# Optimization experiments

Hardware: AMD Instinct MI355X
Metric: run time of the kernel (lower is better)

## Reference

```python
import jax, jax.numpy as jnp
import numpy as np

K = 8                      # batch_k
NONZERO_CUTOFF = 1.4       # nonzero_loss_cutoff
MARGIN = 1.0               # F.triplet_margin_loss default (module's margin arg is unused)
PD_EPS = 1e-6              # torch pairwise_distance eps


def setup_inputs() -> dict:
    key = jax.random.key(0)
    x = jax.random.normal(key, (4096, 128), dtype=jnp.float32)
    return {"x": x}


def _sample_indices(x, key):
    """Distance-weighted negative sampling; returns (a_idx, p_idx, n_idx), each [n*(K-1)]."""
    n, d = x.shape
    # per-row L2 normalize (eps added to norm, as in original)
    xn = x / (jnp.sqrt(jnp.sum(x * x, axis=1, keepdims=True)) + 1e-5)
    # pairwise euclidean distance; identity added under sqrt exactly as original
    sq = jnp.sum(xn * xn, axis=1, keepdims=True)               # [n,1]
    dist2 = sq + sq.T - 2.0 * (xn @ xn.T)                       # [n,n]
    dist = jnp.sqrt(dist2 + jnp.eye(n, dtype=x.dtype))          # [n,n]
    # distance-weighted sampling log-weights (Wu et al.)
    log_w = (2.0 - d) * jnp.log(dist) - (d - 3) / 2.0 * jnp.log(1.0 - 0.25 * dist * dist)
    w = jnp.exp(log_w - jnp.max(log_w))
    # block mask: same-block pairs excluded
    block = jnp.arange(n) // K                                  # [n]
    mask = (block[:, None] != block[None, :]).astype(x.dtype)
    w = w * mask * (dist < NONZERO_CUTOFF).astype(x.dtype)
    row_sum = jnp.sum(w, axis=1, keepdims=True)
    # rows where weights are degenerate fall back to uniform (original's try/except)
    valid = jnp.isfinite(row_sum) & (row_sum > 0) & jnp.all(jnp.isfinite(w), axis=1, keepdims=True)
    logits = jnp.where(valid, jnp.where(w > 0, jnp.log(w), -jnp.inf), 0.0)   # [n,n]
    # batched categorical sampling via Gumbel-max: K-1 negatives per anchor
    g = jax.random.gumbel(key, (n, K - 1, n), dtype=jnp.float32)
    n_idx = jnp.argmax(logits[:, None, :] + g, axis=-1).reshape(-1)          # [n*(K-1)]
    # anchor/positive pairs: for each i, all other members of its block
    r = jnp.arange(n) % K                                       # position in block
    off = jnp.arange(K - 1)
    p_off = jnp.where(off[None, :] < r[:, None], off[None, :], off[None, :] + 1)
    p_idx = (block[:, None] * K + p_off).reshape(-1)            # [n*(K-1)]
    a_idx = jnp.repeat(jnp.arange(n), K - 1)                    # [n*(K-1)]
    return a_idx, p_idx, n_idx


def reference(x) -> jnp.ndarray:
    key = jax.random.key(42)
    a_idx, p_idx, n_idx = _sample_indices(x, key)
    a, p, ng = x[a_idx], x[p_idx], x[n_idx]
    d_ap = jnp.sqrt(jnp.sum((a - p + PD_EPS) ** 2, axis=1))
    d_an = jnp.sqrt(jnp.sum((a - ng + PD_EPS) ** 2, axis=1))
    return jnp.mean(jnp.maximum(d_ap - d_an + MARGIN, 0.0))
```

## Files before the change

kernel.cpp:

```cpp
#include <hip/hip_runtime.h>
#include <stdint.h>

#define NROWS 4096
#define DIM   128
#define KB    8
#define NS    7
#define TCH   16
#define NSEG  4
#define NPAIR 2048
#define HALF_CNT 58720256u

typedef __bf16 v8bf __attribute__((ext_vector_type(8)));
typedef float  v4f  __attribute__((ext_vector_type(4)));

__device__ __forceinline__ uint32_t rotl32(uint32_t x, int r) {
    return (x << r) | (x >> (32 - r));
}

__device__ __forceinline__ void threefry2x32(uint32_t c0, uint32_t c1,
                                             uint32_t& o0, uint32_t& o1) {
    const uint32_t ks0 = 0u;
    const uint32_t ks1 = 42u;
    const uint32_t ks2 = 0x1BD11BDAu ^ ks0 ^ ks1;
    uint32_t x0 = c0 + ks0;
    uint32_t x1 = c1 + ks1;
#define TF_R(r) { x0 += x1; x1 = rotl32(x1, r); x1 ^= x0; }
    TF_R(13) TF_R(15) TF_R(26) TF_R(6)
    x0 += ks1; x1 += ks2 + 1u;
    TF_R(17) TF_R(29) TF_R(16) TF_R(24)
    x0 += ks2; x1 += ks0 + 2u;
    TF_R(13) TF_R(15) TF_R(26) TF_R(6)
    x0 += ks0; x1 += ks1 + 3u;
    TF_R(17) TF_R(29) TF_R(16) TF_R(24)
    x0 += ks1; x1 += ks2 + 4u;
    TF_R(13) TF_R(15) TF_R(26) TF_R(6)
    x0 += ks2; x1 += ks0 + 5u;
#undef TF_R
    o0 = x0; o1 = x1;
}

__device__ __forceinline__ float gumbel_of(uint32_t b) {
    float f = __uint_as_float((b >> 9) | 0x3f800000u) - 1.0f;
    float u = f + 1.17549435e-38f;
    float l1 = __log2f(u);
    float inner = -0.69314718055994531f * l1;
    float l2 = __log2f(inner);
    return -0.69314718055994531f * l2;
}

__global__ void knorm(const float* __restrict__ x, __bf16* __restrict__ xb,
                      float* __restrict__ sqv) {
    const int i = blockIdx.x;
    const int t = threadIdx.x;
    float2 v = ((const float2*)(x + (size_t)i * DIM))[t];
    float s = v.x * v.x + v.y * v.y;
#pragma unroll
    for (int m = 32; m > 0; m >>= 1) s += __shfl_xor(s, m, 64);
    float norm = sqrtf(s) + 1e-5f;
    float ox = v.x / norm, oy = v.y / norm;
    union { __bf16 b[2]; uint32_t u; } ph;
    ph.b[0] = (__bf16)ox; ph.b[1] = (__bf16)oy;
    ((uint32_t*)xb)[i * 64 + t] = ph.u;
    float s2 = ox * ox + oy * oy;
#pragma unroll
    for (int m = 32; m > 0; m >>= 1) s2 += __shfl_xor(s2, m, 64);
    if (t == 0) sqv[i] = s2;
}

__global__ __launch_bounds__(256, 4) void kdist(
        const __bf16* __restrict__ xb, const float* __restrict__ sqv,
        int* __restrict__ cnt, unsigned short* __restrict__ t16,
        float2* __restrict__ nwp) {
    const int lane  = threadIdx.x & 63;
    const int chunk = (blockIdx.x << 2) + (threadIdx.x >> 6);
    const int grp   = blockIdx.y;
    const int rlo = lane & 15;
    const int khi = lane >> 4;
    const unsigned int below = (1u << rlo) - 1u;

    const int afr = grp * 8 + (rlo >> 1) + ((rlo & 1) << 11);
    v8bf ah[4];
#pragma unroll
    for (int ks = 0; ks < 4; ++ks)
        ah[ks] = *(const v8bf*)(xb + (size_t)afr * DIM + ks * 32 + khi * 8);

    const int base = grp * 8 + khi * 2;
    float sqA[4];
    sqA[0] = sqv[base];
    sqA[1] = sqv[base + 2048];
    sqA[2] = sqv[base + 1];
    sqA[3] = sqv[base + 2049];

    const int rbA = ((base)     * 16 + chunk) << 8;
    const int rbB = ((base + 1) * 16 + chunk) << 8;
    unsigned int cA = 0, cB = 0;

    const int tcol0 = chunk * 256 + rlo;

    v8bf bhn[4];
    float sqn;
    {
        const size_t boff = (size_t)tcol0 * DIM + khi * 8;
#pragma unroll
        for (int ks = 0; ks < 4; ++ks) bhn[ks] = *(const v8bf*)(xb + boff + ks * 32);
        sqn = sqv[tcol0];
    }

#pragma unroll 1
    for (int cg = 0; cg < 16; ++cg) {
        v8bf bhc[4];
#pragma unroll
        for (int ks = 0; ks < 4; ++ks) bhc[ks] = bhn[ks];
        const float sqB = sqn;
        const int tcol = tcol0 + cg * 16;

        if (cg < 15) {
            const size_t boff = (size_t)(tcol + 16) * DIM + khi * 8;
#pragma unroll
            for (int ks = 0; ks < 4; ++ks) bhn[ks] = *(const v8bf*)(xb + boff + ks * 32);
            sqn = sqv[tcol + 16];
        }

        v4f acc = {0.f, 0.f, 0.f, 0.f};
#pragma unroll
        for (int ks = 0; ks < 4; ++ks)
            acc = __builtin_amdgcn_mfma_f32_16x16x32_bf16(ah[ks], bhc[ks], acc, 0, 0, 0);

        const int tBlk = tcol >> 3;
        const bool bd0 = (tBlk != grp);
        const bool bd1 = (tBlk != grp + 256);

        float nw[4];
        bool  ic[4];
#pragma unroll
        for (int q = 0; q < 4; ++q) {
            float d2  = fmaf(-2.0f, acc[q], sqA[q] + sqB);
            float l1  = __log2f(d2);
            float t2  = fmaf(-0.25f, d2, 1.0f);
            float l2  = __log2f(t2);
            float wiv = exp2f(fmaf(63.0f, l1, 62.5f * l2));
            bool incl = (d2 < 1.96f) && ((q & 1) ? bd1 : bd0);
            ic[q] = incl;
            nw[q] = incl ? -wiv : -INFINITY;
        }

        const bool uA = ic[0] | ic[1];
        const bool uB = ic[2] | ic[3];
        unsigned long long ballA = __ballot(uA);
        unsigned long long ballB = __ballot(uB);
        unsigned int subA = (unsigned int)((ballA >> (khi * 16)) & 0xFFFFull);
        unsigned int subB = (unsigned int)((ballB >> (khi * 16)) & 0xFFFFull);
        if (uA) {
            int slot = rbA + (int)cA + __popc(subA & below);
            t16[slot] = (unsigned short)tcol;
            nwp[slot] = make_float2(nw[0], nw[1]);
        }
        if (uB) {
            int slot = rbB + (int)cB + __popc(subB & below);
            t16[slot] = (unsigned short)tcol;
            nwp[slot] = make_float2(nw[2], nw[3]);
        }
        cA += (unsigned int)__popc(subA);
        cB += (unsigned int)__popc(subB);
    }

    if (rlo == 0) {
        cnt[base * 16 + chunk]       = (int)cA;
        cnt[(base + 1) * 16 + chunk] = (int)cB;
    }
}

#define TFR4(r)                                                         \
    _Pragma("unroll") for (int k = 0; k < 4; ++k) {                     \
        x0[k] += x1[k]; x1[k] = rotl32(x1[k], (r)); x1[k] ^= x0[k];     \
    }
#define INJ4(a, b)                                                      \
    _Pragma("unroll") for (int k = 0; k < 4; ++k) {                     \
        x0[k] += (a); x1[k] += (b);                                     \
    }

__global__ __launch_bounds__(256, 4) void kgum(
        const int* __restrict__ cnt, const unsigned short* __restrict__ t16,
        const float2* __restrict__ nwp,
        float* __restrict__ pV, int* __restrict__ pI) {
    const int p    = blockIdx.x;
    const int tid  = threadIdx.x;
    const int seg  = tid >> 6;
    const int lane = tid & 63;
    const int j    = lane & 7;
    const int eo   = lane >> 3;
    const bool jv  = (j < 7);
    const uint32_t pb = ((uint32_t)p * 7u + (uint32_t)j) << 12;

    float bkA = INFINITY, bkB = INFINITY;
    int   btA = 0x7FFFFFFF, btB = 0x7FFFFFFF;

#pragma unroll 1
    for (int c = seg * 4; c < seg * 4 + 4; ++c) {
        const int n  = cnt[p * 16 + c];
        const int rb = (p * 16 + c) << 8;
        int e = eo;

#pragma unroll 1
        for (; e + 24 < n; e += 32) {
            uint32_t tt[4];
            float2   nw[4];
#pragma unroll
            for (int k = 0; k < 4; ++k) {
                tt[k] = t16[rb + e + 8 * k];
                nw[k] = nwp[rb + e + 8 * k];
            }
            uint32_t x0[4], x1[4];
#pragma unroll
            for (int k = 0; k < 4; ++k) {
                uint32_t L = pb + tt[k];
                x0[k] = L;
                x1[k] = L + (HALF_CNT + 42u);
            }
            TFR4(13) TFR4(15) TFR4(26) TFR4(6)
            INJ4(42u, 0x1BD11BF0u + 1u)
            TFR4(17) TFR4(29) TFR4(16) TFR4(24)
            INJ4(0x1BD11BF0u, 2u)
            TFR4(13) TFR4(15) TFR4(26) TFR4(6)
            INJ4(0u, 45u)
            TFR4(17) TFR4(29) TFR4(16) TFR4(24)
            INJ4(42u, 0x1BD11BF0u + 4u)
            TFR4(13) TFR4(15) TFR4(26) TFR4(6)
            INJ4(0x1BD11BF0u, 5u)
#pragma unroll
            for (int k = 0; k < 4; ++k) {
                float fA = __uint_as_float((x0[k] >> 9) | 0x3f800000u) - 1.0f;
                float fB = __uint_as_float((x1[k] >> 9) | 0x3f800000u) - 1.0f;
                float l1A = __log2f(fA + 1.17549435e-38f);
                float l1B = __log2f(fB + 1.17549435e-38f);
                float kA = jv ? l1A * nw[k].x : INFINITY;
                float kB = jv ? l1B * nw[k].y : INFINITY;
                const int ti = (int)tt[k];
                if (kA < bkA || (kA == bkA && ti < btA)) { bkA = kA; btA = ti; }
                if (kB < bkB || (kB == bkB && ti < btB)) { bkB = kB; btB = ti; }
            }
        }

#pragma unroll 1
        for (; e < n; e += 8) {
            const uint32_t t = t16[rb + e];
            const float2 nw  = nwp[rb + e];
            const uint32_t L = pb + t;
            uint32_t o0, o1;
            threefry2x32(L, L + HALF_CNT, o0, o1);
            float fA = __uint_as_float((o0 >> 9) | 0x3f800000u) - 1.0f;
            float fB = __uint_as_float((o1 >> 9) | 0x3f800000u) - 1.0f;
            float l1A = __log2f(fA + 1.17549435e-38f);
            float l1B = __log2f(fB + 1.17549435e-38f);
            float kA = jv ? l1A * nw.x : INFINITY;
            float kB = jv ? l1B * nw.y : INFINITY;
            const int ti = (int)t;
            if (kA < bkA || (kA == bkA && ti < btA)) { bkA = kA; btA = ti; }
            if (kB < bkB || (kB == bkB && ti < btB)) { bkB = kB; btB = ti; }
        }
    }

#pragma unroll
    for (int m = 8; m < 64; m <<= 1) {
        float v2 = __shfl_xor(bkA, m, 64);
        int   t2 = __shfl_xor(btA, m, 64);
        if (v2 < bkA || (v2 == bkA && t2 < btA)) { bkA = v2; btA = t2; }
        v2 = __shfl_xor(bkB, m, 64);
        t2 = __shfl_xor(btB, m, 64);
        if (v2 < bkB || (v2 == bkB && t2 < btB)) { bkB = v2; btB = t2; }
    }

    if (lane < NS) {
        size_t s0 = ((size_t)p * NS + lane) * NSEG + seg;
        pV[s0] = bkA; pI[s0] = btA;
        size_t s1 = ((size_t)(p + 2048) * NS + lane) * NSEG + seg;
        pV[s1] = bkB; pI[s1] = btB;
    }
}

__global__ void kcombine(const float* __restrict__ pV, const int* __restrict__ pI,
                         int* __restrict__ nidx, int nc) {
    int s = blockIdx.x * 256 + threadIdx.x;
    if (s >= NROWS * NS) return;
    float bv = INFINITY;
    int bi = 0x7FFFFFFF;
    for (int c = 0; c < nc; ++c) {
        float v = pV[(size_t)s * nc + c];
        int idx = pI[(size_t)s * nc + c];
        if (v < bv || (v == bv && idx < bi)) { bv = v; bi = idx; }
    }
    nidx[s] = (bv == INFINITY) ? -1 : bi;
}

__global__ __launch_bounds__(256, 2) void ksample(
        const __bf16* __restrict__ xb, const float* __restrict__ sqv,
        float* __restrict__ pV, int* __restrict__ pI) {
    const int lane  = threadIdx.x & 63;
    const int chunk = (blockIdx.x << 2) + (threadIdx.x >> 6);
    const int grp   = blockIdx.y;
    const int rlo = lane & 15;
    const int khi = lane >> 4;

    const int afr = grp * 8 + (rlo >> 1) + ((rlo & 1) << 11);
    v8bf ah[4];
#pragma unroll
    for (int ks = 0; ks < 4; ++ks)
        ah[ks] = *(const v8bf*)(xb + (size_t)afr * DIM + ks * 32 + khi * 8);
    const int base = grp * 8 + khi * 2;
    float sqA[4];
    sqA[0] = sqv[base];
    sqA[1] = sqv[base + 2048];
    sqA[2] = sqv[base + 1];
    sqA[3] = sqv[base + 2049];
    const uint32_t P0 = (uint32_t)base;
    const uint32_t P1 = (uint32_t)(base + 1);

    float    bestV[4][NS];
    uint32_t bestP[4];
#pragma unroll
    for (int q = 0; q < 4; ++q) {
        bestP[q] = 0u;
#pragma unroll
        for (int j = 0; j < NS; ++j) bestV[q][j] = INFINITY;
    }
    const int tcol0 = chunk * 256 + rlo;

    v8bf bhn[4];
    float sqn;
    {
        const size_t boff = (size_t)tcol0 * DIM + khi * 8;
#pragma unroll
        for (int ks = 0; ks < 4; ++ks) bhn[ks] = *(const v8bf*)(xb + boff + ks * 32);
        sqn = sqv[tcol0];
    }

#pragma unroll 1
    for (int cg = 0; cg < 16; ++cg) {
        v8bf bhc[4];
#pragma unroll
        for (int ks = 0; ks < 4; ++ks) bhc[ks] = bhn[ks];
        const float sqB = sqn;
        const int tcol = tcol0 + cg * 16;
        if (cg < 15) {
            const size_t boff = (size_t)(tcol + 16) * DIM + khi * 8;
#pragma unroll
            for (int ks = 0; ks < 4; ++ks) bhn[ks] = *(const v8bf*)(xb + boff + ks * 32);
            sqn = sqv[tcol + 16];
        }
        v4f acc = {0.f, 0.f, 0.f, 0.f};
#pragma unroll
        for (int ks = 0; ks < 4; ++ks)
            acc = __builtin_amdgcn_mfma_f32_16x16x32_bf16(ah[ks], bhc[ks], acc, 0, 0, 0);
        const int tBlk = tcol >> 3;
        const bool bd0 = (tBlk != grp);
        const bool bd1 = (tBlk != grp + 256);
        float nw[4];
#pragma unroll
        for (int q = 0; q < 4; ++q) {
            float d2  = fmaf(-2.0f, acc[q], sqA[q] + sqB);
            float l1  = __log2f(d2);
            float t2  = fmaf(-0.25f, d2, 1.0f);
            float l2  = __log2f(t2);
            float wiv = exp2f(fmaf(63.0f, l1, 62.5f * l2));
            bool incl = (d2 < 1.96f) && ((q & 1) ? bd1 : bd0);
            nw[q] = incl ? -wiv : -INFINITY;
        }
        const uint32_t tB = (uint32_t)tcol;
#pragma unroll
        for (int j = 0; j < NS; ++j) {
            uint32_t L0 = ((P0 * 7u + (uint32_t)j) << 12) + tB;
            uint32_t L1 = ((P1 * 7u + (uint32_t)j) << 12) + tB;
            uint32_t o0, o1, o2, o3;
            threefry2x32(L0, L0 + HALF_CNT, o0, o1);
            threefry2x32(L1, L1 + HALF_CNT, o2, o3);
            float vv[4];
            vv[0] = __log2f(__uint_as_float((o0 >> 9) | 0x3f800000u) - 1.0f + 1.17549435e-38f) * nw[0];
            vv[1] = __log2f(__uint_as_float((o1 >> 9) | 0x3f800000u) - 1.0f + 1.17549435e-38f) * nw[1];
            vv[2] = __log2f(__uint_as_float((o2 >> 9) | 0x3f800000u) - 1.0f + 1.17549435e-38f) * nw[2];
            vv[3] = __log2f(__uint_as_float((o3 >> 9) | 0x3f800000u) - 1.0f + 1.17549435e-38f) * nw[3];
            const uint32_t keep = ~(0xFu << (4 * j));
            const uint32_t put  = ((uint32_t)cg) << (4 * j);
#pragma unroll
            for (int q = 0; q < 4; ++q) {
                bool lt = vv[q] < bestV[q][j];
                uint32_t np = (bestP[q] & keep) | put;
                bestV[q][j] = lt ? vv[q] : bestV[q][j];
                bestP[q]    = lt ? np : bestP[q];
            }
        }
    }
#pragma unroll
    for (int q = 0; q < 4; ++q) {
        const int a = base + (q >> 1) + ((q & 1) << 11);
#pragma unroll
        for (int j = 0; j < NS; ++j) {
            float v = bestV[q][j];
            int idx = tcol0 + (int)((bestP[q] >> (4 * j)) & 0xFu) * 16;
#pragma unroll
            for (int m = 1; m < 16; m <<= 1) {
                float v2 = __shfl_xor(v, m, 16);
                int   i2 = __shfl_xor(idx, m, 16);
                if (v2 < v || (v2 == v && i2 < idx)) { v = v2; idx = i2; }
            }
            if (rlo == 0) {
                size_t s = ((size_t)a * NS + j) * TCH + chunk;
                pV[s] = v;
                pI[s] = idx;
            }
        }
    }
}

__global__ void kfixup(int* __restrict__ nidx) {
    const int i = blockIdx.x;
    if (nidx[(size_t)i * NS] >= 0) return;
    const int lane = threadIdx.x;
    for (int j = 0; j < NS; ++j) {
        float bv = -INFINITY;
        int bi = 0x7FFFFFFF;
        for (int t = lane; t < NROWS; t += 64) {
            uint32_t o0, o1;
            float g;
            if (i < 2048) {
                uint32_t L = (((uint32_t)(i * NS + j)) << 12) + (uint32_t)t;
                threefry2x32(L, L + HALF_CNT, o0, o1);
                g = gumbel_of(o0);
            } else {
                uint32_t L = (((uint32_t)((i - 2048) * NS + j)) << 12) + (uint32_t)t;
                threefry2x32(L, L + HALF_CNT, o0, o1);
                g = gumbel_of(o1);
            }
            if (g > bv) { bv = g; bi = t; }
        }
#pragma unroll
        for (int m = 1; m < 64; m <<= 1) {
            float v2 = __shfl_xor(bv, m, 64);
            int   i2 = __shfl_xor(bi, m, 64);
            if (v2 > bv || (v2 == bv && i2 < bi)) { bv = v2; bi = i2; }
        }
        if (lane == 0) nidx[i * NS + j] = bi;
    }
}

__global__ void kloss(const float* __restrict__ x, const int* __restrict__ nidx,
                      float* __restrict__ loss) {
    int s = blockIdx.x * 256 + threadIdx.x;
    if (s >= NROWS * NS) return;
    int i = s / NS, j = s - i * NS;
    int r = i & (KB - 1), blk = i >> 3;
    int po = (j < r) ? j : j + 1;
    int p = blk * KB + po;
    int n = nidx[s] & (NROWS - 1);
    const float4* A  = (const float4*)(x + (size_t)i * DIM);
    const float4* P  = (const float4*)(x + (size_t)p * DIM);
    const float4* Ng = (const float4*)(x + (size_t)n * DIM);
    float sap = 0.0f, san = 0.0f;
#pragma unroll 8
    for (int k = 0; k < DIM / 4; ++k) {
        float4 a = A[k], pv = P[k], nv = Ng[k];
        float d;
        d = a.x - pv.x + 1e-6f; sap += d * d;
        d = a.y - pv.y + 1e-6f; sap += d * d;
        d = a.z - pv.z + 1e-6f; sap += d * d;
        d = a.w - pv.w + 1e-6f; sap += d * d;
        d = a.x - nv.x + 1e-6f; san += d * d;
        d = a.y - nv.y + 1e-6f; san += d * d;
        d = a.z - nv.z + 1e-6f; san += d * d;
        d = a.w - nv.w + 1e-6f; san += d * d;
    }
    loss[s] = fmaxf(sqrtf(sap) - sqrtf(san) + 1.0f, 0.0f);
}

__global__ void kreduce(const float* __restrict__ loss, float* __restrict__ out) {
    __shared__ float part[4];
    const int tid = threadIdx.x;
    float sum = 0.0f;
    for (int s = tid; s < NROWS * NS; s += 256) sum += loss[s];
#pragma unroll
    for (int m = 32; m > 0; m >>= 1) sum += __shfl_xor(sum, m, 64);
    if ((tid & 63) == 0) part[tid >> 6] = sum;
    __syncthreads();
    if (tid == 0) out[0] = (part[0] + part[1] + part[2] + part[3]) / 28672.0f;
}

extern "C" void kernel_launch(void* const* d_in, const int* in_sizes, int n_in,
                              void* d_out, int out_size, void* d_ws, size_t ws_size,
                              hipStream_t stream) {
    const float* x = (const float*)d_in[0];
    float* out = (float*)d_out;

    uint8_t* w = (uint8_t*)d_ws;
    size_t off = 0;
    auto take = [&](size_t bytes) {
        void* p = w + off;
        off = (off + bytes + 255) & ~(size_t)255;
        return p;
    };
    __bf16* xb   = (__bf16*)take((size_t)NROWS * DIM * 2);
    float*  sqv  = (float*)take((size_t)NROWS * 4);
    int*    nidx = (int*)take((size_t)NROWS * NS * 4);
    float*  loss = (float*)take((size_t)NROWS * NS * 4);
    int*    cnt  = (int*)take((size_t)NPAIR * 16 * 4);
    const size_t prefix = off;
    const size_t t16_b = (size_t)NPAIR * 16 * 256 * 2;
    const size_t nwp_b = (size_t)NPAIR * 16 * 256 * 8;
    const size_t pv4_b = (size_t)NROWS * NS * NSEG * 4;
    const size_t NEED_BIG = prefix + ((t16_b + 255) & ~(size_t)255)
                          + ((nwp_b + 255) & ~(size_t)255)
                          + 2 * ((pv4_b + 255) & ~(size_t)255);

    knorm<<<NROWS, 64, 0, stream>>>(x, xb, sqv);

    if (ws_size >= NEED_BIG) {
        unsigned short* t16 = (unsigned short*)take(t16_b);
        float2*         nwp = (float2*)take(nwp_b);
        float*          pV  = (float*)take(pv4_b);
        int*            pI  = (int*)take(pv4_b);
        kdist<<<dim3(TCH / 4, 256), 256, 0, stream>>>(xb, sqv, cnt, t16, nwp);
        kgum<<<NPAIR, 256, 0, stream>>>(cnt, t16, nwp, pV, pI);
        kcombine<<<(NROWS * NS + 255) / 256, 256, 0, stream>>>(pV, pI, nidx, NSEG);
    } else {
        float* pV = (float*)take((size_t)NROWS * NS * TCH * 4);
        int*   pI = (int*)take((size_t)NROWS * NS * TCH * 4);
        ksample<<<dim3(TCH / 4, 256), 256, 0, stream>>>(xb, sqv, pV, pI);
        kcombine<<<(NROWS * NS + 255) / 256, 256, 0, stream>>>(pV, pI, nidx, TCH);
    }

    kfixup<<<NROWS, 64, 0, stream>>>(nidx);
    kloss<<<(NROWS * NS + 255) / 256, 256, 0, stream>>>(x, nidx, loss);
    kreduce<<<1, 256, 0, stream>>>(loss, out);
}
```

Before: 206.7 us.

## Split Gumbel sampling to one wave per chunk with prefetch and LDS reduction

The Gumbel-max kernel now assigns one wavefront to each (pair, chunk) instead of one wavefront looping over four chunks, launching four times more blocks. Each block reduces its four waves' winners through shared memory before writing one partial per chunk group. The unrolled 4-way threefry batch is replaced by a simple loop that prefetches the next element, and the launch bound is raised to 8 blocks per CU. The aim is better load balance and occupancy over the variable-length compacted lists, at the cost of less instruction-level parallelism per thread and an added block sync.

```diff
diff --git a/kernel.cpp b/kernel.cpp
--- a/kernel.cpp
+++ b/kernel.cpp
@@ -170,94 +170,49 @@
     }
 }
 
-#define TFR4(r)                                                         \
-    _Pragma("unroll") for (int k = 0; k < 4; ++k) {                     \
-        x0[k] += x1[k]; x1[k] = rotl32(x1[k], (r)); x1[k] ^= x0[k];     \
-    }
-#define INJ4(a, b)                                                      \
-    _Pragma("unroll") for (int k = 0; k < 4; ++k) {                     \
-        x0[k] += (a); x1[k] += (b);                                     \
-    }
-
-__global__ __launch_bounds__(256, 4) void kgum(
+__global__ __launch_bounds__(256, 8) void kgum(
         const int* __restrict__ cnt, const unsigned short* __restrict__ t16,
         const float2* __restrict__ nwp,
         float* __restrict__ pV, int* __restrict__ pI) {
-    const int p    = blockIdx.x;
-    const int tid  = threadIdx.x;
-    const int seg  = tid >> 6;
-    const int lane = tid & 63;
+    const int wid  = threadIdx.x >> 6;
+    const int rid  = (blockIdx.x << 2) + wid;
+    const int p    = rid >> 4;
+    const int lane = threadIdx.x & 63;
     const int j    = lane & 7;
     const int eo   = lane >> 3;
     const bool jv  = (j < 7);
     const uint32_t pb = ((uint32_t)p * 7u + (uint32_t)j) << 12;
 
+    const int n  = cnt[rid];
+    const int rb = rid << 8;
+
     float bkA = INFINITY, bkB = INFINITY;
     int   btA = 0x7FFFFFFF, btB = 0x7FFFFFFF;
 
+    uint32_t tcur = 0;
+    float2   nwcur = make_float2(0.f, 0.f);
+    if (eo < n) { tcur = t16[rb + eo]; nwcur = nwp[rb + eo]; }
+
 #pragma unroll 1
-    for (int c = seg * 4; c < seg * 4 + 4; ++c) {
-        const int n  = cnt[p * 16 + c];
-        const int rb = (p * 16 + c) << 8;
-        int e = eo;
-
-#pragma unroll 1
-        for (; e + 24 < n; e += 32) {
-            uint32_t tt[4];
-            float2   nw[4];
-#pragma unroll
-            for (int k = 0; k < 4; ++k) {
-                tt[k] = t16[rb + e + 8 * k];
-                nw[k] = nwp[rb + e + 8 * k];
-            }
-            uint32_t x0[4], x1[4];
-#pragma unroll
-            for (int k = 0; k < 4; ++k) {
-                uint32_t L = pb + tt[k];
-                x0[k] = L;
-                x1[k] = L + (HALF_CNT + 42u);
-            }
-            TFR4(13) TFR4(15) TFR4(26) TFR4(6)
-            INJ4(42u, 0x1BD11BF0u + 1u)
-            TFR4(17) TFR4(29) TFR4(16) TFR4(24)
-            INJ4(0x1BD11BF0u, 2u)
-            TFR4(13) TFR4(15) TFR4(26) TFR4(6)
-            INJ4(0u, 45u)
-            TFR4(17) TFR4(29) TFR4(16) TFR4(24)
-            INJ4(42u, 0x1BD11BF0u + 4u)
-            TFR4(13) TFR4(15) TFR4(26) TFR4(6)
-            INJ4(0x1BD11BF0u, 5u)
-#pragma unroll
-            for (int k = 0; k < 4; ++k) {
-                float fA = __uint_as_float((x0[k] >> 9) | 0x3f800000u) - 1.0f;
-                float fB = __uint_as_float((x1[k] >> 9) | 0x3f800000u) - 1.0f;
-                float l1A = __log2f(fA + 1.17549435e-38f);
-                float l1B = __log2f(fB + 1.17549435e-38f);
-                float kA = jv ? l1A * nw[k].x : INFINITY;
-                float kB = jv ? l1B * nw[k].y : INFINITY;
-                const int ti = (int)tt[k];
-                if (kA < bkA || (kA == bkA && ti < btA)) { bkA = kA; btA = ti; }
-                if (kB < bkB || (kB == bkB && ti < btB)) { bkB = kB; btB = ti; }
-            }
-        }
-
-#pragma unroll 1
-        for (; e < n; e += 8) {
-            const uint32_t t = t16[rb + e];
-            const float2 nw  = nwp[rb + e];
-            const uint32_t L = pb + t;
-            uint32_t o0, o1;
-            threefry2x32(L, L + HALF_CNT, o0, o1);
-            float fA = __uint_as_float((o0 >> 9) | 0x3f800000u) - 1.0f;
-            float fB = __uint_as_float((o1 >> 9) | 0x3f800000u) - 1.0f;
-            float l1A = __log2f(fA + 1.17549435e-38f);
-            float l1B = __log2f(fB + 1.17549435e-38f);
-            float kA = jv ? l1A * nw.x : INFINITY;
-            float kB = jv ? l1B * nw.y : INFINITY;
-            const int ti = (int)t;
-            if (kA < bkA || (kA == bkA && ti < btA)) { bkA = kA; btA = ti; }
-            if (kB < bkB || (kB == bkB && ti < btB)) { bkB = kB; btB = ti; }
-        }
+    for (int e = eo; e < n; e += 8) {
+        uint32_t tnx = tcur;
+        float2   nwnx = nwcur;
+        if (e + 8 < n) { tnx = t16[rb + e + 8]; nwnx = nwp[rb + e + 8]; }
+
+        const uint32_t L = pb + tcur;
+        uint32_t o0, o1;
+        threefry2x32(L, L + HALF_CNT, o0, o1);
+        float fA = __uint_as_float((o0 >> 9) | 0x3f800000u) - 1.0f;
+        float fB = __uint_as_float((o1 >> 9) | 0x3f800000u) - 1.0f;
+        float l1A = __log2f(fA + 1.17549435e-38f);
+        float l1B = __log2f(fB + 1.17549435e-38f);
+        float kA = jv ? l1A * nwcur.x : INFINITY;
+        float kB = jv ? l1B * nwcur.y : INFINITY;
+        const int ti = (int)tcur;
+        if (kA < bkA || (kA == bkA && ti < btA)) { bkA = kA; btA = ti; }
+        if (kB < bkB || (kB == bkB && ti < btB)) { bkB = kB; btB = ti; }
+
+        tcur = tnx; nwcur = nwnx;
     }
 
 #pragma unroll
@@ -270,11 +225,26 @@
         if (v2 < bkB || (v2 == bkB && t2 < btB)) { bkB = v2; btB = t2; }
     }
 
+    __shared__ float sV[4][2][NS];
+    __shared__ int   sT[4][2][NS];
     if (lane < NS) {
-        size_t s0 = ((size_t)p * NS + lane) * NSEG + seg;
-        pV[s0] = bkA; pI[s0] = btA;
-        size_t s1 = ((size_t)(p + 2048) * NS + lane) * NSEG + seg;
-        pV[s1] = bkB; pI[s1] = btB;
+        sV[wid][0][lane] = bkA; sT[wid][0][lane] = btA;
+        sV[wid][1][lane] = bkB; sT[wid][1][lane] = btB;
+    }
+    __syncthreads();
+    if (threadIdx.x < 2 * NS) {
+        const int r = threadIdx.x / NS, jj = threadIdx.x - r * NS;
+        float v = sV[0][r][jj];
+        int   t = sT[0][r][jj];
+#pragma unroll
+        for (int w = 1; w < 4; ++w) {
+            float v2 = sV[w][r][jj];
+            int   t2 = sT[w][r][jj];
+            if (v2 < v || (v2 == v && t2 < t)) { v = v2; t = t2; }
+        }
+        const int cgrp = blockIdx.x & 3;
+        size_t s = ((size_t)(p + r * 2048) * NS + jj) * NSEG + cgrp;
+        pV[s] = v; pI[s] = t;
     }
 }
 
@@ -517,7 +487,7 @@
         float*          pV  = (float*)take(pv4_b);
         int*            pI  = (int*)take(pv4_b);
         kdist<<<dim3(TCH / 4, 256), 256, 0, stream>>>(xb, sqv, cnt, t16, nwp);
-        kgum<<<NPAIR, 256, 0, stream>>>(cnt, t16, nwp, pV, pI);
+        kgum<<<NPAIR * 16 / 4, 256, 0, stream>>>(cnt, t16, nwp, pV, pI);
         kcombine<<<(NROWS * NS + 255) / 256, 256, 0, stream>>>(pV, pI, nidx, NSEG);
     } else {
         float* pV = (float*)take((size_t)NROWS * NS * TCH * 4);
```

Measured after the change: 202.0 us. -2.3%, faster.
